# Performance work log

Hardware: AMD Instinct MI355X
Metric: run time of the kernel (lower is better)

Reference implementation:

```python
import jax, jax.numpy as jnp
import numpy as np

B, S, D, H = 2, 2048, 256, 8


def setup_inputs() -> dict:
    key = jax.random.key(0)
    ks = jax.random.split(key, 9)
    s = 1.0 / np.sqrt(D)
    x = jax.random.normal(ks[0], (B, S, D), dtype=jnp.float32)
    Wq = jax.random.normal(ks[1], (H, D, D), dtype=jnp.float32) * s
    Wk = jax.random.normal(ks[2], (H, D, D), dtype=jnp.float32) * s
    Wv = jax.random.normal(ks[3], (H, D, D), dtype=jnp.float32) * s
    bq = jnp.zeros((H, D), dtype=jnp.float32)
    bk = jnp.zeros((H, D), dtype=jnp.float32)
    bv = jnp.zeros((H, D), dtype=jnp.float32)
    Wo = jax.random.normal(ks[4], (H * D, D), dtype=jnp.float32) * (1.0 / np.sqrt(H * D))
    bo = jnp.zeros((D,), dtype=jnp.float32)
    return {"x": x, "Wq": Wq, "bq": bq, "Wk": Wk, "bk": bk, "Wv": Wv, "bv": bv, "Wo": Wo, "bo": bo}


def reference(x, Wq, bq, Wk, bk, Wv, bv, Wo, bo):
    # Per-head Q/K/V projections, batched over heads via einsum.
    # q,k,v: [B, H, S, D]
    q = jnp.einsum('bsd,hde->bhse', x, Wq) + bq[None, :, None, :]
    k = jnp.einsum('bsd,hde->bhse', x, Wk) + bk[None, :, None, :]
    v = jnp.einsum('bsd,hde->bhse', x, Wv) + bv[None, :, None, :]
    scale = 1.0 / jnp.sqrt(jnp.asarray(D, dtype=x.dtype))
    scores = jnp.einsum('bhse,bhte->bhst', q, k) * scale  # [B,H,S,S]
    attn = jax.nn.softmax(scores, axis=-1)
    o = jnp.einsum('bhst,bhte->bhse', attn, v)  # [B,H,S,D]
    # Concat heads along feature dim: [B,S,H*D]
    concat = o.transpose(0, 2, 1, 3).reshape(B, S, H * D)
    return concat @ Wo + bo
```

## Files before the change

### kernel.cpp

```cpp
#include <hip/hip_runtime.h>

typedef __bf16 bf16x8 __attribute__((ext_vector_type(8)));
typedef __bf16 bf16x4 __attribute__((ext_vector_type(4)));
typedef float  f32x4  __attribute__((ext_vector_type(4)));
typedef float  f32x16 __attribute__((ext_vector_type(16)));

#define DEVI __device__ __forceinline__

DEVI bf16x8 ld8(const __bf16* p) { return *reinterpret_cast<const bf16x8*>(p); }
DEVI f32x4 mfma16(bf16x8 a, bf16x8 b, f32x4 c) {
  return __builtin_amdgcn_mfma_f32_16x16x32_bf16(a, b, c, 0, 0, 0);
}
DEVI f32x16 mfma32(bf16x8 a, bf16x8 b, f32x16 c) {
  return __builtin_amdgcn_mfma_f32_32x32x16_bf16(a, b, c, 0, 0, 0);
}
DEVI void gl_lds16(const void* g, void* l) {
  __builtin_amdgcn_global_load_lds((__attribute__((address_space(1))) void*)g,
                                   (__attribute__((address_space(3))) void*)l, 16, 0, 0);
}
DEVI unsigned pk2(float a, float b) {
  union { __bf16 h[2]; unsigned u; } x;
  x.h[0] = (__bf16)a; x.h[1] = (__bf16)b; return x.u;
}

#if __has_builtin(__builtin_amdgcn_exp2f)
#define EXP2(x) __builtin_amdgcn_exp2f(x)
#else
#define EXP2(x) exp2f(x)
#endif

__global__ __launch_bounds__(256) void k_prep(
    const float* __restrict__ x, const float* __restrict__ Wq,
    const float* __restrict__ Wk, const float* __restrict__ Wv,
    const float* __restrict__ Wo, __bf16* __restrict__ xb,
    __bf16* __restrict__ Wt, __bf16* __restrict__ Woh, __bf16* __restrict__ Wol) {
  const int bid = blockIdx.x;
  if (bid < 1024) {
    const int i = bid * 256 + threadIdx.x;
    f32x4 v = reinterpret_cast<const f32x4*>(x)[i];
    bf16x4 o;
    o[0] = (__bf16)v[0]; o[1] = (__bf16)v[1]; o[2] = (__bf16)v[2]; o[3] = (__bf16)v[3];
    reinterpret_cast<bf16x4*>(xb)[i] = o;
    return;
  }
  __shared__ float t[32][33];
  const int flat = bid - 1024;
  const float* in; __bf16* oh; __bf16* ol = nullptr;
  int R, C, c0, r0;
  bool lo = false;
  if (flat < 1536) {
    const int which = flat >> 9, rem = flat & 511;
    const int h = rem >> 6, tt = rem & 63;
    c0 = (tt & 7) * 32; r0 = (tt >> 3) * 32;
    const float* Wsrc = which == 0 ? Wq : which == 1 ? Wk : Wv;
    in = Wsrc + h * 65536;
    oh = Wt + which * 524288 + h * 65536;
    R = 256; C = 256;
  } else {
    const int rem = flat - 1536;
    c0 = (rem & 7) * 32; r0 = (rem >> 3) * 32;
    in = Wo; oh = Woh; ol = Wol; lo = true;
    R = 2048; C = 256;
  }
  const int tx = threadIdx.x & 31, ty = threadIdx.x >> 5;
  #pragma unroll
  for (int k = 0; k < 32; k += 8)
    t[ty + k][tx] = in[(size_t)(r0 + ty + k) * C + c0 + tx];
  __syncthreads();
  #pragma unroll
  for (int k = 0; k < 32; k += 8) {
    const float v = t[tx][ty + k];
    const size_t o = (size_t)(c0 + ty + k) * R + r0 + tx;
    const __bf16 h = (__bf16)v;
    oh[o] = h;
    if (lo) ol[o] = (__bf16)(v - (float)h);
  }
}

__global__ __launch_bounds__(256) void k_qkv(
    const __bf16* __restrict__ xb, const __bf16* __restrict__ Wt,
    const float* __restrict__ bq, const float* __restrict__ bk, const float* __restrict__ bv,
    __bf16* __restrict__ Qb, __bf16* __restrict__ Kb, __bf16* __restrict__ Vtb) {
  const int wl = threadIdx.x >> 6, lane = threadIdx.x & 63;
  const int g = lane >> 4, qc = lane & 15;
  const int which = blockIdx.z >> 3, h = blockIdx.z & 7;
  const int sblk = blockIdx.x * 256;
  const int s0 = sblk + wl * 64;
  const int e0 = blockIdx.y * 64;
  const __bf16* Wm = Wt + ((size_t)blockIdx.z << 16);
  const float* bias = (which == 0 ? bq : which == 1 ? bk : bv) + h * 256;
  const int b = sblk >> 11;
  const int bh = b * 8 + h;
  const int sm0 = s0 & 2047;
  f32x4 acc[4][4] = {};

  if (which == 2) {
    #pragma unroll
    for (int kk = 0; kk < 8; kk++) {
      bf16x8 af[4], bf[4];
      #pragma unroll
      for (int ai = 0; ai < 4; ai++)
        af[ai] = ld8(xb + (size_t)(s0 + ai * 16 + qc) * 256 + kk * 32 + g * 8);
      #pragma unroll
      for (int bj = 0; bj < 4; bj++)
        bf[bj] = ld8(Wm + (size_t)(e0 + bj * 16 + qc) * 256 + kk * 32 + g * 8);
      #pragma unroll
      for (int ai = 0; ai < 4; ai++)
        #pragma unroll
        for (int bj = 0; bj < 4; bj++)
          acc[ai][bj] = mfma16(af[ai], bf[bj], acc[ai][bj]);
    }
    #pragma unroll
    for (int bj = 0; bj < 4; bj++) {
      const int e = e0 + bj * 16 + qc;
      const float be = bias[e];
      #pragma unroll
      for (int ai = 0; ai < 4; ai++) {
        bf16x4 pk;
        #pragma unroll
        for (int r = 0; r < 4; r++) pk[r] = (__bf16)(acc[ai][bj][r] + be);
        *reinterpret_cast<bf16x4*>(Vtb + ((size_t)(bh * 256 + e)) * 2048 +
                                   sm0 + ai * 16 + g * 4) = pk;
      }
    }
  } else {
    #pragma unroll
    for (int kk = 0; kk < 8; kk++) {
      bf16x8 af[4], bf[4];
      #pragma unroll
      for (int ai = 0; ai < 4; ai++)
        af[ai] = ld8(Wm + (size_t)(e0 + ai * 16 + qc) * 256 + kk * 32 + g * 8);
      #pragma unroll
      for (int bj = 0; bj < 4; bj++)
        bf[bj] = ld8(xb + (size_t)(s0 + bj * 16 + qc) * 256 + kk * 32 + g * 8);
      #pragma unroll
      for (int ai = 0; ai < 4; ai++)
        #pragma unroll
        for (int bj = 0; bj < 4; bj++)
          acc[ai][bj] = mfma16(af[ai], bf[bj], acc[ai][bj]);
    }
    const float sc = (which == 0) ? 0.0625f * 1.4426950408889634f : 1.0f;
    __bf16* Out = (which == 0) ? Qb : Kb;
    float be[4][4];
    #pragma unroll
    for (int ai = 0; ai < 4; ai++)
      #pragma unroll
      for (int r = 0; r < 4; r++) be[ai][r] = bias[e0 + ai * 16 + g * 4 + r];
    #pragma unroll
    for (int ai = 0; ai < 4; ai++)
      #pragma unroll
      for (int bj = 0; bj < 4; bj++) {
        const int srow = sm0 + bj * 16 + qc;
        bf16x4 pk;
        #pragma unroll
        for (int r = 0; r < 4; r++)
          pk[r] = (__bf16)((acc[ai][bj][r] + be[ai][r]) * sc);
        *reinterpret_cast<bf16x4*>(Out + ((size_t)(bh * 2048 + srow)) * 256 +
                                   e0 + ai * 16 + g * 4) = pk;
      }
  }
}

__global__ __launch_bounds__(256) void k_attn(
    const __bf16* __restrict__ Qb, const __bf16* __restrict__ Kb,
    const __bf16* __restrict__ Vtb, __bf16* __restrict__ Oh, __bf16* __restrict__ Ol) {
  __shared__ __align__(16) unsigned char smem[131072];
  const int tid = threadIdx.x;
  const int wl = tid >> 6, lane = tid & 63;
  const int hi = lane >> 5, q = lane & 31;

  const int bid = blockIdx.x;
  const int s = (bid & 7) * 32 + (bid >> 3);
  const int bh = s >> 4, qt = s & 15;

  const int q0w = qt * 128 + wl * 32;
  const char* Kg = (const char*)Kb + ((size_t)bh * 2048) * 512;
  const char* Vg = (const char*)Vtb + (size_t)bh * 256 * 4096;
  const __bf16* Qp = Qb + ((size_t)(bh * 2048 + q0w + q)) * 256;

  bf16x8 qf[16];
  #pragma unroll
  for (int kk = 0; kk < 16; kk++) qf[kk] = ld8(Qp + kk * 16 + hi * 8);

  f32x16 acc[8];
  #pragma unroll
  for (int i = 0; i < 8; i++)
    #pragma unroll
    for (int e = 0; e < 16; e++) acc[i][e] = 0.f;

  auto stage = [&](int nb, int t) {
    unsigned char* kbp = smem + nb * 32768 + wl * 8192;
    unsigned char* vbp = smem + 65536 + nb * 32768 + wl * 8192;
    #pragma unroll
    for (int j = 0; j < 8; j++) {
      const int O = wl * 8192 + j * 1024 + lane * 16;
      const int kv = O >> 9;
      const int c = ((O >> 4) & 31) ^ (kv & 15);
      gl_lds16(Kg + (size_t)t * 32768 + (size_t)kv * 512 + c * 16, kbp + j * 1024);
    }
    #pragma unroll
    for (int j = 0; j < 8; j++) {
      const int O = wl * 8192 + j * 1024 + lane * 16;
      const int sb = O >> 10;
      const int kvh = (O >> 9) & 1;
      const int dlo = (O >> 6) & 7;
      const int ci = (O >> 4) & 3;
      const int d = sb * 8 + dlo;
      gl_lds16(Vg + (size_t)d * 4096 + (size_t)t * 128 + kvh * 64 + ((ci ^ (sb & 3)) << 4),
               vbp + j * 1024);
    }
  };

  float m_run = -3.0e38f, l_run = 0.f;
  stage(0, 0);
  __syncthreads();

  for (int t = 0; t < 32; t++) {
    const int cur = t & 1;
    const unsigned char* kbc = smem + cur * 32768;
    const unsigned char* vbc = smem + 65536 + cur * 32768;
    if (t < 31) stage(cur ^ 1, t + 1);

    f32x16 st0, st1;
    #pragma unroll
    for (int e = 0; e < 16; e++) { st0[e] = 0.f; st1[e] = 0.f; }
    __builtin_amdgcn_s_setprio(1);
    #pragma unroll
    for (int kk = 0; kk < 16; kk++) {
      const int o0 = q * 512 + ((((kk << 1) + hi) ^ (q & 15)) << 4);
      bf16x8 k0 = *reinterpret_cast<const bf16x8*>(kbc + o0);
      bf16x8 k1 = *reinterpret_cast<const bf16x8*>(kbc + o0 + 16384);
      st0 = mfma32(k0, qf[kk], st0);
      st1 = mfma32(k1, qf[kk], st1);
    }
    __builtin_amdgcn_s_setprio(0);

    f32x16 mx;
    #pragma unroll
    for (int r = 0; r < 16; r++) mx[r] = fmaxf(st0[r], st1[r]);
    #pragma unroll
    for (int w2 = 8; w2 > 0; w2 >>= 1)
      #pragma unroll
      for (int r = 0; r < w2; r++) mx[r] = fmaxf(mx[r], mx[r + w2]);
    const float rmax = fmaxf(mx[0], __shfl_xor(mx[0], 32));
    if (__any(rmax > m_run + 8.0f)) {
      const float m_new = fmaxf(rmax, m_run);
      const float alpha = EXP2(m_run - m_new);
      m_run = m_new;
      l_run *= alpha;
      #pragma unroll
      for (int r = 0; r < 16; r++) {
        const float ar = __shfl(alpha, (r & 3) + 8 * (r >> 2) + 4 * hi);
        #pragma unroll
        for (int dt = 0; dt < 8; dt++) acc[dt][r] *= ar;
      }
    }
    f32x16 sm_;
    #pragma unroll
    for (int r = 0; r < 16; r++) {
      st0[r] = EXP2(st0[r] - m_run);
      st1[r] = EXP2(st1[r] - m_run);
      sm_[r] = st0[r] + st1[r];
    }
    #pragma unroll
    for (int w2 = 8; w2 > 0; w2 >>= 1)
      #pragma unroll
      for (int r = 0; r < w2; r++) sm_[r] += sm_[r + w2];
    l_run += sm_[0] + __shfl_xor(sm_[0], 32);

    bf16x8 pa[4];
    #define MKCHUNK(STV, H2, OUT) {                          \
      const unsigned L0 = pk2(STV[H2 * 8 + 0], STV[H2 * 8 + 1]);  \
      const unsigned L1 = pk2(STV[H2 * 8 + 2], STV[H2 * 8 + 3]);  \
      const unsigned H0 = pk2(STV[H2 * 8 + 4], STV[H2 * 8 + 5]);  \
      const unsigned H1 = pk2(STV[H2 * 8 + 6], STV[H2 * 8 + 7]);  \
      const unsigned xL0 = __shfl_xor(L0, 32), xL1 = __shfl_xor(L1, 32); \
      const unsigned xH0 = __shfl_xor(H0, 32), xH1 = __shfl_xor(H1, 32); \
      unsigned pw[4];                                        \
      pw[0] = hi ? xH0 : L0;  pw[1] = hi ? xH1 : L1;         \
      pw[2] = hi ? H0 : xL0;  pw[3] = hi ? H1 : xL1;         \
      OUT = *reinterpret_cast<bf16x8*>(pw); }
    MKCHUNK(st0, 0, pa[0]); MKCHUNK(st0, 1, pa[1]);
    MKCHUNK(st1, 0, pa[2]); MKCHUNK(st1, 1, pa[3]);
    #undef MKCHUNK

    __builtin_amdgcn_s_setprio(1);
    #pragma unroll
    for (int dt = 0; dt < 8; dt++) {
      const int d = dt * 32 + q;
      const int base = (d >> 3) * 1024 + (d & 7) * 64;
      const int key = (d >> 3) & 3;
      #pragma unroll
      for (int c = 0; c < 4; c++) {
        const int off = base + (c >> 1) * 512 +
                        (((((c & 1) << 1) | hi) ^ key) << 4);
        bf16x8 vf = *reinterpret_cast<const bf16x8*>(vbc + off);
        acc[dt] = mfma32(pa[c], vf, acc[dt]);
      }
    }
    __builtin_amdgcn_s_setprio(0);
    __syncthreads();
  }

  float linv[16];
  #pragma unroll
  for (int r = 0; r < 16; r++)
    linv[r] = 1.f / __shfl(l_run, (r & 3) + 8 * (r >> 2) + 4 * hi);
  const int b = bh >> 3, h = bh & 7;
  #pragma unroll
  for (int dt = 0; dt < 8; dt++) {
    #pragma unroll
    for (int r = 0; r < 16; r++) {
      const float v = acc[dt][r] * linv[r];
      const int qrow = (r & 3) + 8 * (r >> 2) + 4 * hi;
      const size_t off = (size_t)b * (2048 * 2048) +
                         (size_t)(q0w + qrow) * 2048 + h * 256 + dt * 32 + q;
      const __bf16 hv = (__bf16)v;
      Oh[off] = hv;
      Ol[off] = (__bf16)(v - (float)hv);
    }
  }
}

__global__ __launch_bounds__(256) void k_out(
    const __bf16* __restrict__ Oh, const __bf16* __restrict__ Ol,
    const __bf16* __restrict__ Wh, const __bf16* __restrict__ Wl,
    const float* __restrict__ bo, float* __restrict__ out) {
  const int w = threadIdx.x >> 6, lane = threadIdx.x & 63;
  const int g = lane >> 4, qc = lane & 15;
  const int m0 = blockIdx.x * 64 + w * 16, n0 = blockIdx.y * 64;
  const int k0 = blockIdx.z * 1024;
  f32x4 acc[4] = {};
  const __bf16* ah_p = Oh + (size_t)(m0 + qc) * 2048 + k0 + g * 8;
  const __bf16* al_p = Ol + (size_t)(m0 + qc) * 2048 + k0 + g * 8;
  for (int kk = 0; kk < 32; kk++) {
    bf16x8 ah = ld8(ah_p + kk * 32);
    bf16x8 al = ld8(al_p + kk * 32);
    #pragma unroll
    for (int nt = 0; nt < 4; nt++) {
      const size_t nrow = (size_t)(n0 + nt * 16 + qc) * 2048 + k0 + kk * 32 + g * 8;
      bf16x8 bh = ld8(Wh + nrow);
      bf16x8 bl = ld8(Wl + nrow);
      acc[nt] = mfma16(ah, bh, acc[nt]);
      acc[nt] = mfma16(al, bh, acc[nt]);
      acc[nt] = mfma16(ah, bl, acc[nt]);
    }
  }
  #pragma unroll
  for (int nt = 0; nt < 4; nt++) {
    const int n = n0 + nt * 16 + qc;
    const float bb = (blockIdx.z == 0) ? bo[n] : 0.f;
    #pragma unroll
    for (int r = 0; r < 4; r++)
      unsafeAtomicAdd(&out[(m0 + g * 4 + r) * 256 + n], acc[nt][r] + bb);
  }
}

extern "C" void kernel_launch(void* const* d_in, const int* in_sizes, int n_in,
                              void* d_out, int out_size, void* d_ws, size_t ws_size,
                              hipStream_t stream) {
  const float* x  = (const float*)d_in[0];
  const float* Wq = (const float*)d_in[1];
  const float* bq = (const float*)d_in[2];
  const float* Wk = (const float*)d_in[3];
  const float* bk = (const float*)d_in[4];
  const float* Wv = (const float*)d_in[5];
  const float* bv = (const float*)d_in[6];
  const float* Wo = (const float*)d_in[7];
  const float* bo = (const float*)d_in[8];
  char* p = (char*)d_ws;
  __bf16* xb  = (__bf16*)(p);
  __bf16* Wt  = (__bf16*)(p + (2ull  << 20));
  __bf16* Woh = (__bf16*)(p + (5ull  << 20));
  __bf16* Wol = (__bf16*)(p + (6ull  << 20));
  __bf16* Qb  = (__bf16*)(p + (7ull  << 20));
  __bf16* Kb  = (__bf16*)(p + (23ull << 20));
  __bf16* Vtb = (__bf16*)(p + (39ull << 20));
  __bf16* Ohb = (__bf16*)(p + (55ull << 20));
  __bf16* Olb = (__bf16*)(p + (71ull << 20));

  k_prep<<<dim3(3072), dim3(256), 0, stream>>>(x, Wq, Wk, Wv, Wo, xb, Wt, Woh, Wol);
  k_qkv<<<dim3(16, 4, 24), dim3(256), 0, stream>>>(xb, Wt, bq, bk, bv, Qb, Kb, Vtb);
  k_attn<<<dim3(256), dim3(256), 0, stream>>>(Qb, Kb, Vtb, Ohb, Olb);
  (void)hipMemsetAsync(d_out, 0, (size_t)out_size * sizeof(float), stream);
  k_out<<<dim3(64, 4, 2), dim3(256), 0, stream>>>(Ohb, Olb, Woh, Wol, bo, (float*)d_out);
}
```

Before: 255.4 us.

## Software-pipeline QK^T of next tile with softmax and PV of current tile

Restructures the flash-attention loop so the QK^T MFMAs for tile t+1 are issued before the softmax and PV work for tile t, using two ping-pong score register sets. K and V staging are split so the next K tile is loaded while the current tile's PV runs, with V staging issued after a barrier. The aim is to hide softmax latency and LDS loads behind matrix work. The cost is an extra 32 score registers per lane and more barriers, which may lower occupancy or cause spills.

```diff
diff --git a/kernel.cpp b/kernel.cpp
--- a/kernel.cpp
+++ b/kernel.cpp
@@ -188,9 +188,8 @@
     #pragma unroll
     for (int e = 0; e < 16; e++) acc[i][e] = 0.f;
 
-  auto stage = [&](int nb, int t) {
+  auto stageK = [&](int nb, int t) {
     unsigned char* kbp = smem + nb * 32768 + wl * 8192;
-    unsigned char* vbp = smem + 65536 + nb * 32768 + wl * 8192;
     #pragma unroll
     for (int j = 0; j < 8; j++) {
       const int O = wl * 8192 + j * 1024 + lane * 16;
@@ -198,6 +197,9 @@
       const int c = ((O >> 4) & 31) ^ (kv & 15);
       gl_lds16(Kg + (size_t)t * 32768 + (size_t)kv * 512 + c * 16, kbp + j * 1024);
     }
+  };
+  auto stageV = [&](int nb, int t) {
+    unsigned char* vbp = smem + 65536 + nb * 32768 + wl * 8192;
     #pragma unroll
     for (int j = 0; j < 8; j++) {
       const int O = wl * 8192 + j * 1024 + lane * 16;
@@ -212,95 +214,123 @@
   };
 
   float m_run = -3.0e38f, l_run = 0.f;
-  stage(0, 0);
+
+  #define QK_PHASE(P, S0, S1) {                                            \
+    const unsigned char* kbc = smem + (P) * 32768;                         \
+    _Pragma("unroll")                                                      \
+    for (int e = 0; e < 16; e++) { S0[e] = 0.f; S1[e] = 0.f; }             \
+    __builtin_amdgcn_s_setprio(1);                                         \
+    _Pragma("unroll")                                                      \
+    for (int kk = 0; kk < 16; kk++) {                                      \
+      const int o0 = q * 512 + ((((kk << 1) + hi) ^ (q & 15)) << 4);       \
+      bf16x8 k0 = *reinterpret_cast<const bf16x8*>(kbc + o0);              \
+      bf16x8 k1 = *reinterpret_cast<const bf16x8*>(kbc + o0 + 16384);      \
+      S0 = mfma32(k0, qf[kk], S0);                                         \
+      S1 = mfma32(k1, qf[kk], S1);                                         \
+    }                                                                      \
+    __builtin_amdgcn_s_setprio(0);                                         \
+  }
+
+  #define OLD_PHASE(P, S0, S1) {                                           \
+    f32x16 mx;                                                             \
+    _Pragma("unroll")                                                      \
+    for (int r = 0; r < 16; r++) mx[r] = fmaxf(S0[r], S1[r]);              \
+    _Pragma("unroll")                                                      \
+    for (int w2 = 8; w2 > 0; w2 >>= 1)                                     \
+      _Pragma("unroll")                                                    \
+      for (int r = 0; r < w2; r++) mx[r] = fmaxf(mx[r], mx[r + w2]);       \
+    const float rmax = fmaxf(mx[0], __shfl_xor(mx[0], 32));                \
+    if (__any(rmax > m_run + 8.0f)) {                                      \
+      const float m_new = fmaxf(rmax, m_run);                              \
+      const float alpha = EXP2(m_run - m_new);                             \
+      m_run = m_new;                                                       \
+      l_run *= alpha;                                                      \
+      _Pragma("unroll")                                                    \
+      for (int r = 0; r < 16; r++) {                                       \
+        const float ar = __shfl(alpha, (r & 3) + 8 * (r >> 2) + 4 * hi);   \
+        _Pragma("unroll")                                                  \
+        for (int dt = 0; dt < 8; dt++) acc[dt][r] *= ar;                   \
+      }                                                                    \
+    }                                                                      \
+    f32x16 sm_;                                                            \
+    _Pragma("unroll")                                                      \
+    for (int r = 0; r < 16; r++) {                                         \
+      S0[r] = EXP2(S0[r] - m_run);                                         \
+      S1[r] = EXP2(S1[r] - m_run);                                         \
+      sm_[r] = S0[r] + S1[r];                                              \
+    }                                                                      \
+    _Pragma("unroll")                                                      \
+    for (int w2 = 8; w2 > 0; w2 >>= 1)                                     \
+      _Pragma("unroll")                                                    \
+      for (int r = 0; r < w2; r++) sm_[r] += sm_[r + w2];                  \
+    l_run += sm_[0] + __shfl_xor(sm_[0], 32);                              \
+    bf16x8 pa[4];                                                          \
+    MKCHUNK(S0, 0, pa[0]); MKCHUNK(S0, 1, pa[1]);                          \
+    MKCHUNK(S1, 0, pa[2]); MKCHUNK(S1, 1, pa[3]);                          \
+    const unsigned char* vbc = smem + 65536 + (P) * 32768;                 \
+    __builtin_amdgcn_s_setprio(1);                                         \
+    _Pragma("unroll")                                                      \
+    for (int dt = 0; dt < 8; dt++) {                                       \
+      const int d = dt * 32 + q;                                           \
+      const int base = (d >> 3) * 1024 + (d & 7) * 64;                     \
+      const int key = (d >> 3) & 3;                                        \
+      _Pragma("unroll")                                                    \
+      for (int c = 0; c < 4; c++) {                                        \
+        const int off = base + (c >> 1) * 512 +                            \
+                        (((((c & 1) << 1) | hi) ^ key) << 4);              \
+        bf16x8 vf = *reinterpret_cast<const bf16x8*>(vbc + off);           \
+        acc[dt] = mfma32(pa[c], vf, acc[dt]);                              \
+      }                                                                    \
+    }                                                                      \
+    __builtin_amdgcn_s_setprio(0);                                         \
+  }
+
+  #define MKCHUNK(STV, H2, OUT) {                                          \
+    const unsigned L0 = pk2(STV[H2 * 8 + 0], STV[H2 * 8 + 1]);             \
+    const unsigned L1 = pk2(STV[H2 * 8 + 2], STV[H2 * 8 + 3]);             \
+    const unsigned H0 = pk2(STV[H2 * 8 + 4], STV[H2 * 8 + 5]);             \
+    const unsigned H1 = pk2(STV[H2 * 8 + 6], STV[H2 * 8 + 7]);             \
+    const unsigned xL0 = __shfl_xor(L0, 32), xL1 = __shfl_xor(L1, 32);     \
+    const unsigned xH0 = __shfl_xor(H0, 32), xH1 = __shfl_xor(H1, 32);     \
+    unsigned pw[4];                                                        \
+    pw[0] = hi ? xH0 : L0;  pw[1] = hi ? xH1 : L1;                         \
+    pw[2] = hi ? H0 : xL0;  pw[3] = hi ? H1 : xL1;                         \
+    OUT = *reinterpret_cast<bf16x8*>(pw); }
+
+  f32x16 sA0, sA1, sB0, sB1;
+
+  stageK(0, 0); stageV(0, 0);
   __syncthreads();
-
-  for (int t = 0; t < 32; t++) {
-    const int cur = t & 1;
-    const unsigned char* kbc = smem + cur * 32768;
-    const unsigned char* vbc = smem + 65536 + cur * 32768;
-    if (t < 31) stage(cur ^ 1, t + 1);
-
-    f32x16 st0, st1;
-    #pragma unroll
-    for (int e = 0; e < 16; e++) { st0[e] = 0.f; st1[e] = 0.f; }
-    __builtin_amdgcn_s_setprio(1);
-    #pragma unroll
-    for (int kk = 0; kk < 16; kk++) {
-      const int o0 = q * 512 + ((((kk << 1) + hi) ^ (q & 15)) << 4);
-      bf16x8 k0 = *reinterpret_cast<const bf16x8*>(kbc + o0);
-      bf16x8 k1 = *reinterpret_cast<const bf16x8*>(kbc + o0 + 16384);
-      st0 = mfma32(k0, qf[kk], st0);
-      st1 = mfma32(k1, qf[kk], st1);
-    }
-    __builtin_amdgcn_s_setprio(0);
-
-    f32x16 mx;
-    #pragma unroll
-    for (int r = 0; r < 16; r++) mx[r] = fmaxf(st0[r], st1[r]);
-    #pragma unroll
-    for (int w2 = 8; w2 > 0; w2 >>= 1)
-      #pragma unroll
-      for (int r = 0; r < w2; r++) mx[r] = fmaxf(mx[r], mx[r + w2]);
-    const float rmax = fmaxf(mx[0], __shfl_xor(mx[0], 32));
-    if (__any(rmax > m_run + 8.0f)) {
-      const float m_new = fmaxf(rmax, m_run);
-      const float alpha = EXP2(m_run - m_new);
-      m_run = m_new;
-      l_run *= alpha;
-      #pragma unroll
-      for (int r = 0; r < 16; r++) {
-        const float ar = __shfl(alpha, (r & 3) + 8 * (r >> 2) + 4 * hi);
-        #pragma unroll
-        for (int dt = 0; dt < 8; dt++) acc[dt][r] *= ar;
-      }
-    }
-    f32x16 sm_;
-    #pragma unroll
-    for (int r = 0; r < 16; r++) {
-      st0[r] = EXP2(st0[r] - m_run);
-      st1[r] = EXP2(st1[r] - m_run);
-      sm_[r] = st0[r] + st1[r];
-    }
-    #pragma unroll
-    for (int w2 = 8; w2 > 0; w2 >>= 1)
-      #pragma unroll
-      for (int r = 0; r < w2; r++) sm_[r] += sm_[r + w2];
-    l_run += sm_[0] + __shfl_xor(sm_[0], 32);
-
-    bf16x8 pa[4];
-    #define MKCHUNK(STV, H2, OUT) {                          \
-      const unsigned L0 = pk2(STV[H2 * 8 + 0], STV[H2 * 8 + 1]);  \
-      const unsigned L1 = pk2(STV[H2 * 8 + 2], STV[H2 * 8 + 3]);  \
-      const unsigned H0 = pk2(STV[H2 * 8 + 4], STV[H2 * 8 + 5]);  \
-      const unsigned H1 = pk2(STV[H2 * 8 + 6], STV[H2 * 8 + 7]);  \
-      const unsigned xL0 = __shfl_xor(L0, 32), xL1 = __shfl_xor(L1, 32); \
-      const unsigned xH0 = __shfl_xor(H0, 32), xH1 = __shfl_xor(H1, 32); \
-      unsigned pw[4];                                        \
-      pw[0] = hi ? xH0 : L0;  pw[1] = hi ? xH1 : L1;         \
-      pw[2] = hi ? H0 : xL0;  pw[3] = hi ? H1 : xL1;         \
-      OUT = *reinterpret_cast<bf16x8*>(pw); }
-    MKCHUNK(st0, 0, pa[0]); MKCHUNK(st0, 1, pa[1]);
-    MKCHUNK(st1, 0, pa[2]); MKCHUNK(st1, 1, pa[3]);
-    #undef MKCHUNK
-
-    __builtin_amdgcn_s_setprio(1);
-    #pragma unroll
-    for (int dt = 0; dt < 8; dt++) {
-      const int d = dt * 32 + q;
-      const int base = (d >> 3) * 1024 + (d & 7) * 64;
-      const int key = (d >> 3) & 3;
-      #pragma unroll
-      for (int c = 0; c < 4; c++) {
-        const int off = base + (c >> 1) * 512 +
-                        (((((c & 1) << 1) | hi) ^ key) << 4);
-        bf16x8 vf = *reinterpret_cast<const bf16x8*>(vbc + off);
-        acc[dt] = mfma32(pa[c], vf, acc[dt]);
-      }
-    }
-    __builtin_amdgcn_s_setprio(0);
+  QK_PHASE(0, sA0, sA1);
+  stageK(1, 1);
+  __syncthreads();
+  stageV(1, 1);
+
+  for (int tb = 1; tb < 31; tb += 2) {
     __syncthreads();
-  }
+    QK_PHASE(1, sB0, sB1);
+    stageK(0, tb + 1);
+    OLD_PHASE(0, sA0, sA1);
+    __syncthreads();
+    stageV(0, tb + 1);
+
+    __syncthreads();
+    QK_PHASE(0, sA0, sA1);
+    stageK(1, tb + 2);
+    OLD_PHASE(1, sB0, sB1);
+    __syncthreads();
+    stageV(1, tb + 2);
+  }
+
+  __syncthreads();
+  QK_PHASE(1, sB0, sB1);
+  OLD_PHASE(0, sA0, sA1);
+  __syncthreads();
+  OLD_PHASE(1, sB0, sB1);
+
+  #undef QK_PHASE
+  #undef OLD_PHASE
+  #undef MKCHUNK
 
   float linv[16];
   #pragma unroll
```

Result: slower. 333.0 us (+30.4%).
